# Kernel optimization log

Measured on AMD Instinct MI355X. Metric: run time of the kernel, lower is better.

The kernel has to match this reference:

```python
import jax, jax.numpy as jnp
import numpy as np

_SHAPE = (4, 2, 8, 256, 513)  # N, 2(real/imag), C, T, F


def setup_inputs() -> dict:
    key = jax.random.key(0)
    k1, k2, k3 = jax.random.split(key, 3)
    return {
        "mixture": jax.random.normal(k1, _SHAPE, dtype=jnp.float32),
        "target": jax.random.normal(k2, _SHAPE, dtype=jnp.float32),
        "noise": jax.random.normal(k3, _SHAPE, dtype=jnp.float32),
        "ref_mic_idx": 0,
    }


def _to_complex(x):
    # (N, 2, C, T, F) real-imag stacked -> complex (N, C, T, F)
    return jax.lax.complex(x[:, 0], x[:, 1])


def _mean_spatial_cov(s):
    # s: complex (N, C, T, F) -> time-averaged covariance (N, F, C, C)
    N, C, T, F = s.shape
    sc = jnp.transpose(s, (0, 3, 2, 1))  # (N, F, T, C)
    # outer product V V^H summed over T, fused into one batched GEMM
    return jnp.einsum("nftc,nftd->nfcd", sc, jnp.conj(sc)) / T


def reference(mixture, target, noise, ref_mic_idx):
    y = _to_complex(mixture)  # (N, C, T, F)
    x = _to_complex(target)
    v = _to_complex(noise)
    N, C, T, F = y.shape

    phi_target = _mean_spatial_cov(x)  # (N, F, C, C)
    # diagonal loading: torch adds load to BOTH real and imag parts (RI dim broadcast)
    load = (0.001 / np.sqrt(2)) * (1.0 + 1.0j)
    phi_noise = _mean_spatial_cov(v) + jnp.asarray(load, dtype=y.dtype) * jnp.eye(C, dtype=y.dtype)

    G = jnp.linalg.inv(phi_noise) @ phi_target  # (N, F, C, C)
    l = jnp.trace(G, axis1=-2, axis2=-1)  # (N, F)
    # W = (1/l) * G @ e_ref  -> select column ref_mic_idx
    W = G[..., ref_mic_idx] / l[..., None]  # (N, F, C)

    # X_bf(n,t,f) = W^H y = sum_c conj(W)_{nfc} y_{nctf}
    X_bf = jnp.einsum("nfc,nctf->ntf", jnp.conj(W), y)  # (N, T, F)
    # restack real/imag and add singleton channel dim -> (N, 2, 1, T, F)
    out = jnp.stack([X_bf.real, X_bf.imag], axis=1)[:, :, None]
    return out
```

## Files before the change

### kernel.cpp

```cpp
#include <hip/hip_runtime.h>

#define Nn 4
#define Cc 8
#define Tt 256
#define Ff 513
#define TFs (Tt * Ff)
#define NCHUNK 16
#define TCHUNK (Tt / NCHUNK)

__global__ __launch_bounds__(64) void cov_partial(
    const float* __restrict__ target, const float* __restrict__ noise,
    float* __restrict__ partial)
{
    int f = blockIdx.x * 64 + threadIdx.x;
    if (f >= Ff) return;
    int n = blockIdx.y;
    int z = blockIdx.z;
    int inp = z & 1;
    int chunk = z >> 1;

    const float* src = inp ? noise : target;
    const float* bt = src + (size_t)n * 2 * Cc * TFs + (size_t)(chunk * TCHUNK) * Ff + f;

    float ar[36], ai[36];
#pragma unroll
    for (int p = 0; p < 36; ++p) { ar[p] = 0.f; ai[p] = 0.f; }

#pragma unroll 2
    for (int tt = 0; tt < TCHUNK; ++tt) {
        float re[8], im[8];
#pragma unroll
        for (int c = 0; c < 8; ++c) {
            re[c] = bt[(size_t)c * TFs];
            im[c] = bt[(size_t)(Cc + c) * TFs];
        }
        int p = 0;
#pragma unroll
        for (int a = 0; a < 8; ++a) {
#pragma unroll
            for (int b = a; b < 8; ++b, ++p) {
                ar[p] += re[a] * re[b] + im[a] * im[b];
                if (a != b)
                    ai[p] += im[a] * re[b] - re[a] * im[b];
            }
        }
        bt += Ff;
    }

    float* dst = partial + (((size_t)inp * Nn + n) * NCHUNK + chunk) * 72 * (size_t)Ff + f;
#pragma unroll
    for (int p = 0; p < 36; ++p) {
        dst[(size_t)(2 * p + 0) * Ff] = ar[p];
        dst[(size_t)(2 * p + 1) * Ff] = ai[p];
    }
}

__global__ __launch_bounds__(64) void mvdr_weights(
    const float* __restrict__ partial, const int* __restrict__ ref_ptr,
    float2* __restrict__ wconj)
{
    int f = blockIdx.x;
    int n = blockIdx.y;
    int lane = threadIdx.x;

    __shared__ float cov[144];

    for (int comp = lane; comp < 144; comp += 64) {
        int inp = comp >= 72;
        int idx = inp ? comp - 72 : comp;
        float s = 0.f;
#pragma unroll
        for (int ch = 0; ch < NCHUNK; ++ch)
            s += partial[((((size_t)inp * Nn + n) * NCHUNK + ch) * 72 + idx) * (size_t)Ff + f];
        cov[comp] = s;
    }
    __syncthreads();

    int r = lane >> 3, c = lane & 7;
    int lo = r < c ? r : c, hi = r < c ? c : r;
    int p = lo * 8 - lo * (lo - 1) / 2 + (hi - lo);
    const float invT = 1.0f / (float)Tt;
    const float dl = 0.001f / 1.41421356237309515f;
    float sgn = (r > c) ? -1.f : 1.f;

    float2 a = make_float2(cov[72 + 2 * p] * invT, sgn * cov[72 + 2 * p + 1] * invT);
    float2 b = make_float2(cov[2 * p] * invT,      sgn * cov[2 * p + 1] * invT);
    if (r == c) { a.x += dl; a.y += dl; }

    for (int k = 0; k < 8; ++k) {
        float mag = (c == k && r >= k) ? (a.x * a.x + a.y * a.y) : -1.f;
        int midx = r;
#pragma unroll
        for (int st = 8; st < 64; st <<= 1) {
            float om = __shfl_xor(mag, st, 64);
            int   oi = __shfl_xor(midx, st, 64);
            if (om > mag) { mag = om; midx = oi; }
        }
        int piv = __shfl(midx, k, 64);

        int srcr = (r == k) ? piv : ((r == piv) ? k : r);
        int src = srcr * 8 + c;
        a.x = __shfl(a.x, src, 64); a.y = __shfl(a.y, src, 64);
        b.x = __shfl(b.x, src, 64); b.y = __shfl(b.y, src, 64);

        float pvx = __shfl(a.x, k * 8 + k, 64), pvy = __shfl(a.y, k * 8 + k, 64);
        float d = pvx * pvx + pvy * pvy;
        float ipx = pvx / d, ipy = -pvy / d;
        if (r == k) {
            float2 t = a;
            a = make_float2(t.x * ipx - t.y * ipy, t.x * ipy + t.y * ipx);
            t = b;
            b = make_float2(t.x * ipx - t.y * ipy, t.x * ipy + t.y * ipx);
        }

        float rax = __shfl(a.x, k * 8 + c, 64), ray = __shfl(a.y, k * 8 + c, 64);
        float rbx = __shfl(b.x, k * 8 + c, 64), rby = __shfl(b.y, k * 8 + c, 64);
        float fx  = __shfl(a.x, r * 8 + k, 64), fy  = __shfl(a.y, r * 8 + k, 64);
        if (r != k) {
            a.x -= fx * rax - fy * ray;  a.y -= fx * ray + fy * rax;
            b.x -= fx * rbx - fy * rby;  b.y -= fx * rby + fy * rbx;
        }
    }

    float tx = (r == c) ? b.x : 0.f, ty = (r == c) ? b.y : 0.f;
#pragma unroll
    for (int st = 1; st < 64; st <<= 1) {
        tx += __shfl_xor(tx, st, 64);
        ty += __shfl_xor(ty, st, 64);
    }

    int ref = *ref_ptr;
    if (c == ref) {
        float den = tx * tx + ty * ty;
        float wx = (b.x * tx + b.y * ty) / den;
        float wy = (b.y * tx - b.x * ty) / den;
        wconj[((size_t)n * Ff + f) * 8 + r] = make_float2(wx, -wy);
    }
}

__global__ __launch_bounds__(256) void beamform(
    const float* __restrict__ y, const float2* __restrict__ wconj,
    float* __restrict__ out)
{
    int idx = blockIdx.x * 256 + threadIdx.x;
    int n = idx / TFs;
    int rem = idx - n * TFs;
    int t = rem / Ff;
    int f = rem - t * Ff;

    size_t base_re = (size_t)n * 2 * Cc * TFs + (size_t)t * Ff + f;
    size_t base_im = base_re + (size_t)Cc * TFs;
    const float2* w = wconj + ((size_t)n * Ff + f) * 8;

    float xr = 0.f, xi = 0.f;
#pragma unroll
    for (int c = 0; c < Cc; ++c) {
        float yre = y[base_re + (size_t)c * TFs];
        float yim = y[base_im + (size_t)c * TFs];
        float2 wc = w[c];
        xr += wc.x * yre - wc.y * yim;
        xi += wc.x * yim + wc.y * yre;
    }
    size_t ob = (size_t)n * 2 * TFs + (size_t)t * Ff + f;
    out[ob] = xr;
    out[ob + TFs] = xi;
}

extern "C" void kernel_launch(void* const* d_in, const int* in_sizes, int n_in,
                              void* d_out, int out_size, void* d_ws, size_t ws_size,
                              hipStream_t stream) {
    const float* mixture = (const float*)d_in[0];
    const float* target  = (const float*)d_in[1];
    const float* noise   = (const float*)d_in[2];
    const int*   refp    = (const int*)d_in[3];
    float* out = (float*)d_out;

    float*  partial = (float*)d_ws;
    float2* wconj = (float2*)((char*)d_ws +
                              (size_t)2 * Nn * NCHUNK * 72 * Ff * sizeof(float));

    cov_partial<<<dim3(9, Nn, NCHUNK * 2), 64, 0, stream>>>(target, noise, partial);
    mvdr_weights<<<dim3(Ff, Nn), 64, 0, stream>>>(partial, refp, wconj);
    beamform<<<dim3((Nn * TFs) / 256), 256, 0, stream>>>(mixture, wconj, out);
}
```

Baseline: 170.8 us.

## Store covariance partials frequency-major, double time chunks, reduce directly in registers

The partial-covariance buffer is changed from component-major to frequency-major, so each thread writes its 72 values as contiguous float4 stores. The weights kernel then reads float2 pairs per lane straight into registers instead of going through a shared-memory reduction and barrier. The number of time chunks doubles to give the covariance kernel more parallelism. The trade-off is a workspace twice as large and twice the partial reads in the weights kernel, and the per-thread float4 stores are strided across threads rather than coalesced.

```diff
diff --git a/kernel.cpp b/kernel.cpp
--- a/kernel.cpp
+++ b/kernel.cpp
@@ -5,8 +5,9 @@
 #define Tt 256
 #define Ff 513
 #define TFs (Tt * Ff)
-#define NCHUNK 16
+#define NCHUNK 32
 #define TCHUNK (Tt / NCHUNK)
+#define SLAB ((size_t)Ff * 72)
 
 __global__ __launch_bounds__(64) void cov_partial(
     const float* __restrict__ target, const float* __restrict__ noise,
@@ -47,11 +48,12 @@
         bt += Ff;
     }
 
-    float* dst = partial + (((size_t)inp * Nn + n) * NCHUNK + chunk) * 72 * (size_t)Ff + f;
+    float* dst = partial + (((size_t)inp * Nn + n) * NCHUNK + chunk) * SLAB
+                 + (size_t)f * 72;
 #pragma unroll
-    for (int p = 0; p < 36; ++p) {
-        dst[(size_t)(2 * p + 0) * Ff] = ar[p];
-        dst[(size_t)(2 * p + 1) * Ff] = ai[p];
+    for (int j = 0; j < 18; ++j) {
+        float4 v = make_float4(ar[2 * j], ai[2 * j], ar[2 * j + 1], ai[2 * j + 1]);
+        *(float4*)(dst + 4 * j) = v;
     }
 }
 
@@ -63,28 +65,29 @@
     int n = blockIdx.y;
     int lane = threadIdx.x;
 
-    __shared__ float cov[144];
-
-    for (int comp = lane; comp < 144; comp += 64) {
-        int inp = comp >= 72;
-        int idx = inp ? comp - 72 : comp;
-        float s = 0.f;
-#pragma unroll
-        for (int ch = 0; ch < NCHUNK; ++ch)
-            s += partial[((((size_t)inp * Nn + n) * NCHUNK + ch) * 72 + idx) * (size_t)Ff + f];
-        cov[comp] = s;
-    }
-    __syncthreads();
-
     int r = lane >> 3, c = lane & 7;
     int lo = r < c ? r : c, hi = r < c ? c : r;
     int p = lo * 8 - lo * (lo - 1) / 2 + (hi - lo);
+
+    const float* pT = partial + ((size_t)(0 * Nn + n) * NCHUNK) * SLAB
+                      + (size_t)f * 72 + 2 * p;
+    const float* pN = partial + ((size_t)(1 * Nn + n) * NCHUNK) * SLAB
+                      + (size_t)f * 72 + 2 * p;
+    float2 sT = make_float2(0.f, 0.f), sN = make_float2(0.f, 0.f);
+#pragma unroll
+    for (int ch = 0; ch < NCHUNK; ++ch) {
+        float2 vT = *(const float2*)(pT + ch * SLAB);
+        float2 vN = *(const float2*)(pN + ch * SLAB);
+        sT.x += vT.x; sT.y += vT.y;
+        sN.x += vN.x; sN.y += vN.y;
+    }
+
     const float invT = 1.0f / (float)Tt;
     const float dl = 0.001f / 1.41421356237309515f;
     float sgn = (r > c) ? -1.f : 1.f;
 
-    float2 a = make_float2(cov[72 + 2 * p] * invT, sgn * cov[72 + 2 * p + 1] * invT);
-    float2 b = make_float2(cov[2 * p] * invT,      sgn * cov[2 * p + 1] * invT);
+    float2 a = make_float2(sN.x * invT, sgn * sN.y * invT);
+    float2 b = make_float2(sT.x * invT, sgn * sT.y * invT);
     if (r == c) { a.x += dl; a.y += dl; }
 
     for (int k = 0; k < 8; ++k) {
@@ -177,7 +180,7 @@
 
     float*  partial = (float*)d_ws;
     float2* wconj = (float2*)((char*)d_ws +
-                              (size_t)2 * Nn * NCHUNK * 72 * Ff * sizeof(float));
+                              (size_t)2 * Nn * NCHUNK * SLAB * sizeof(float));
 
     cov_partial<<<dim3(9, Nn, NCHUNK * 2), 64, 0, stream>>>(target, noise, partial);
     mvdr_weights<<<dim3(Ff, Nn), 64, 0, stream>>>(partial, refp, wconj);
```

Result: faster. 156.8 us (-8.2%).

## Accumulate covariance via atomics with finer time chunks, dropping partial-sum reduction

Applied to the files above, without the earlier changes.

Splits the time dimension into 64 chunks instead of 16 so more blocks are launched, and has each block atomically add its covariance sums into one zeroed accumulator instead of writing per-chunk partials. The weights kernel then reads the final sums directly rather than reducing 16 partials through shared memory. This removes the partial-buffer write and read traffic and raises occupancy of the covariance stage. In exchange it adds a memset launch and many float atomics, so summation order becomes nondeterministic.

```diff
diff --git a/kernel.cpp b/kernel.cpp
--- a/kernel.cpp
+++ b/kernel.cpp
@@ -5,22 +5,26 @@
 #define Tt 256
 #define Ff 513
 #define TFs (Tt * Ff)
-#define NCHUNK 16
+#define NCHUNK 64
 #define TCHUNK (Tt / NCHUNK)
+#define ACC_FLOATS ((size_t)2 * Nn * 72 * Ff)
 
-__global__ __launch_bounds__(64) void cov_partial(
+__global__ __launch_bounds__(64, 4) void cov_partial(
     const float* __restrict__ target, const float* __restrict__ noise,
-    float* __restrict__ partial)
+    float* __restrict__ accum)
 {
-    int f = blockIdx.x * 64 + threadIdx.x;
-    if (f >= Ff) return;
+    int lane = threadIdx.x;
+    int f = blockIdx.x * 64 + lane;
+    bool valid = f < Ff;
+    int fc = valid ? f : (Ff - 1);
     int n = blockIdx.y;
     int z = blockIdx.z;
     int inp = z & 1;
     int chunk = z >> 1;
 
     const float* src = inp ? noise : target;
-    const float* bt = src + (size_t)n * 2 * Cc * TFs + (size_t)(chunk * TCHUNK) * Ff + f;
+    const float* bt = src + (size_t)n * 2 * Cc * TFs
+                      + (size_t)(chunk * TCHUNK) * Ff + fc;
 
     float ar[36], ai[36];
 #pragma unroll
@@ -47,44 +51,44 @@
         bt += Ff;
     }
 
-    float* dst = partial + (((size_t)inp * Nn + n) * NCHUNK + chunk) * 72 * (size_t)Ff + f;
+    if (valid) {
+        float* dst = accum + ((size_t)inp * Nn + n) * (72 * (size_t)Ff) + f;
+        int p = 0;
 #pragma unroll
-    for (int p = 0; p < 36; ++p) {
-        dst[(size_t)(2 * p + 0) * Ff] = ar[p];
-        dst[(size_t)(2 * p + 1) * Ff] = ai[p];
+        for (int a = 0; a < 8; ++a) {
+#pragma unroll
+            for (int b = a; b < 8; ++b, ++p) {
+                atomicAdd(dst + (size_t)(2 * p) * Ff, ar[p]);
+                if (a != b)
+                    atomicAdd(dst + (size_t)(2 * p + 1) * Ff, ai[p]);
+            }
+        }
     }
 }
 
 __global__ __launch_bounds__(64) void mvdr_weights(
-    const float* __restrict__ partial, const int* __restrict__ ref_ptr,
+    const float* __restrict__ accum, const int* __restrict__ ref_ptr,
     float2* __restrict__ wconj)
 {
     int f = blockIdx.x;
     int n = blockIdx.y;
     int lane = threadIdx.x;
 
-    __shared__ float cov[144];
-
-    for (int comp = lane; comp < 144; comp += 64) {
-        int inp = comp >= 72;
-        int idx = inp ? comp - 72 : comp;
-        float s = 0.f;
-#pragma unroll
-        for (int ch = 0; ch < NCHUNK; ++ch)
-            s += partial[((((size_t)inp * Nn + n) * NCHUNK + ch) * 72 + idx) * (size_t)Ff + f];
-        cov[comp] = s;
-    }
-    __syncthreads();
-
     int r = lane >> 3, c = lane & 7;
     int lo = r < c ? r : c, hi = r < c ? c : r;
     int p = lo * 8 - lo * (lo - 1) / 2 + (hi - lo);
+
+    const float* PT = accum + ((size_t)0 * Nn + n) * (72 * (size_t)Ff) + f;
+    const float* PN = accum + ((size_t)1 * Nn + n) * (72 * (size_t)Ff) + f;
+    float sTx = PT[(size_t)(2 * p) * Ff], sTy = PT[(size_t)(2 * p + 1) * Ff];
+    float sNx = PN[(size_t)(2 * p) * Ff], sNy = PN[(size_t)(2 * p + 1) * Ff];
+
     const float invT = 1.0f / (float)Tt;
     const float dl = 0.001f / 1.41421356237309515f;
     float sgn = (r > c) ? -1.f : 1.f;
 
-    float2 a = make_float2(cov[72 + 2 * p] * invT, sgn * cov[72 + 2 * p + 1] * invT);
-    float2 b = make_float2(cov[2 * p] * invT,      sgn * cov[2 * p + 1] * invT);
+    float2 a = make_float2(sNx * invT, sgn * sNy * invT);
+    float2 b = make_float2(sTx * invT, sgn * sTy * invT);
     if (r == c) { a.x += dl; a.y += dl; }
 
     for (int k = 0; k < 8; ++k) {
@@ -175,11 +179,11 @@
     const int*   refp    = (const int*)d_in[3];
     float* out = (float*)d_out;
 
-    float*  partial = (float*)d_ws;
-    float2* wconj = (float2*)((char*)d_ws +
-                              (size_t)2 * Nn * NCHUNK * 72 * Ff * sizeof(float));
+    float*  accum = (float*)d_ws;
+    float2* wconj = (float2*)((char*)d_ws + (2 << 20));
 
-    cov_partial<<<dim3(9, Nn, NCHUNK * 2), 64, 0, stream>>>(target, noise, partial);
-    mvdr_weights<<<dim3(Ff, Nn), 64, 0, stream>>>(partial, refp, wconj);
+    hipMemsetAsync(accum, 0, ACC_FLOATS * sizeof(float), stream);
+    cov_partial<<<dim3(9, Nn, NCHUNK * 2), 64, 0, stream>>>(target, noise, accum);
+    mvdr_weights<<<dim3(Ff, Nn), 64, 0, stream>>>(accum, refp, wconj);
     beamform<<<dim3((Nn * TFs) / 256), 256, 0, stream>>>(mixture, wconj, out);
 }
```

Result: slower. 209.4 us (+22.6%).
